# Kernel optimization log

Measured on AMD Instinct MI355X. Metric: run time of the kernel, lower is better.

Reference implementation:

```python
import jax, jax.numpy as jnp
import numpy as np

B = 1024
D = 768          # 2 * hidden_size
HID = 384        # hidden_size (split point for mu/sigma)
MLP_H = 300      # InfoNCE hidden size
LOG2PI = float(np.log(2.0 * np.pi))


def setup_inputs() -> dict:
    key = jax.random.key(0)
    ks = jax.random.split(key, 12)
    s = 0.02
    return {
        "zl": jax.random.normal(ks[0], (B, 20, D), jnp.float32),
        "zv": jax.random.normal(ks[1], (B, 36, D), jnp.float32),
        "fc_l_w": jax.random.normal(ks[2], (20,), jnp.float32) * s,
        "fc_l_b": jax.random.normal(ks[3], (), jnp.float32) * s,
        "fc_v_w": jax.random.normal(ks[4], (36,), jnp.float32) * s,
        "fc_v_b": jax.random.normal(ks[5], (), jnp.float32) * s,
        "W1": jax.random.normal(ks[6], (MLP_H, 2 * HID), jnp.float32) * s,
        "b1": jnp.zeros((MLP_H,), jnp.float32),
        "W2": jax.random.normal(ks[7], (1, MLP_H), jnp.float32) * s,
        "b2": jnp.zeros((1,), jnp.float32),
        "eps1": jax.random.normal(ks[8], (B, HID), jnp.float32),
        "eps2": jax.random.normal(ks[9], (B, HID), jnp.float32),
        "perm": jax.random.permutation(ks[10], B),
    }


def _log_prob(mu, sigma, x):
    # Independent(Normal(mu, sigma), 1).log_prob(x)
    z = (x - mu) / sigma
    return jnp.sum(-jnp.log(sigma) - 0.5 * LOG2PI - 0.5 * z * z, axis=-1)


def reference(zl, zv, fc_l_w, fc_l_b, fc_v_w, fc_v_b, W1, b1, W2, b2, eps1, eps2, perm):
    # fc over token dim: permute(0,2,1) @ Linear(20->1) -> [B, D]
    z1 = jnp.einsum('bsd,s->bd', zl, fc_l_w) + fc_l_b
    z2 = jnp.einsum('bsd,s->bd', zv, fc_v_w) + fc_v_b

    mu1, sig1 = z1[:, :HID], jax.nn.softplus(z1[:, HID:]) + 1e-7
    mu2, sig2 = z2[:, :HID], jax.nn.softplus(z2[:, HID:]) + 1e-7

    # rsample
    s1 = mu1 + sig1 * eps1  # [B, HID]
    s2 = mu2 + sig2 * eps2

    kl_1_2 = _log_prob(mu1, sig1, s1) - _log_prob(mu2, sig2, s1)
    kl_2_1 = _log_prob(mu2, sig2, s2) - _log_prob(mu1, sig1, s2)
    d_skl = jnp.mean(kl_1_2 + kl_2_1) / 2.0

    # InfoNCE(x=s1, y=s2): F(x,y) = softplus(relu([x,y]W1^T + b1) W2^T + b2)
    W1x, W1y = W1[:, :HID], W1[:, HID:]
    Ax = s1 @ W1x.T            # [B, MLP_H], x contribution
    By = s2 @ W1y.T            # [B, MLP_H], y contribution
    w2 = W2[0]                 # [MLP_H]

    # T0: matched pairs
    T0 = jax.nn.softplus(jax.nn.relu(Ax + By + b1) @ w2 + b2[0])  # [B]

    # T1[i, j] = F(x_j, y_perm[i]); tile via broadcasting instead of repeat+cat
    By_p = By[perm]                                             # [B, MLP_H]
    h = jax.nn.relu(Ax[None, :, :] + By_p[:, None, :] + b1)     # [B, B, MLP_H]
    T1 = jax.nn.softplus(h @ w2 + b2[0])                        # [B, B]

    lower_bound = T0.mean() - (jax.scipy.special.logsumexp(T1, axis=1).mean() - jnp.log(jnp.float32(B)))
    return d_skl - lower_bound
```

## Files before the change

### kernel.cpp

```cpp
#include <hip/hip_runtime.h>
#include <math.h>

#define BB   1024
#define DD   768
#define HIDV 384
#define MLPH 300
#define MLPP 320

typedef float v2f __attribute__((ext_vector_type(2)));

__device__ __forceinline__ float softplusf(float x) {
    return (x > 20.f) ? x : log1pf(expf(x));
}

__global__ void k_init(float* __restrict__ ws) {
    int i = blockIdx.x * 256 + threadIdx.x;
    if (i < 16 + BB) ws[i] = 0.f;
}

__global__ __launch_bounds__(192, 3) void k_rs(
    const float* __restrict__ zl, const float* __restrict__ zv,
    const float* __restrict__ wl, const float* __restrict__ blp,
    const float* __restrict__ wv, const float* __restrict__ bvp,
    const float* __restrict__ eps1, const float* __restrict__ eps2,
    float* __restrict__ s1, float* __restrict__ s2, float* __restrict__ accum)
{
    __shared__ float SG[768];
    __shared__ float pr[3];
    int tid = threadIdx.x;
    int b = blockIdx.x;

    const float4* zl4 = (const float4*)(zl + (size_t)b * 15360) + tid;
    const float4* zv4 = (const float4*)(zv + (size_t)b * 27648) + tid;

    float a1[4] = {0.f, 0.f, 0.f, 0.f};
    float a2[4] = {0.f, 0.f, 0.f, 0.f};

    #pragma unroll
    for (int s = 0; s < 20; ++s) {
        float4 v = zl4[s * 192];
        float w = wl[s];
        a1[0] = fmaf(v.x, w, a1[0]);
        a1[1] = fmaf(v.y, w, a1[1]);
        a1[2] = fmaf(v.z, w, a1[2]);
        a1[3] = fmaf(v.w, w, a1[3]);
    }
    #pragma unroll
    for (int s = 0; s < 36; ++s) {
        float4 v = zv4[s * 192];
        float w = wv[s];
        a2[0] = fmaf(v.x, w, a2[0]);
        a2[1] = fmaf(v.y, w, a2[1]);
        a2[2] = fmaf(v.z, w, a2[2]);
        a2[3] = fmaf(v.w, w, a2[3]);
    }

    float bl = blp[0], bv = bvp[0];

    if (tid >= 96) {
        float o1[4], o2[4];
        #pragma unroll
        for (int j = 0; j < 4; ++j) {
            o1[j] = softplusf(a1[j] + bl) + 1e-7f;
            o2[j] = softplusf(a2[j] + bv) + 1e-7f;
        }
        *(float4*)(SG + (tid - 96) * 4)       = make_float4(o1[0], o1[1], o1[2], o1[3]);
        *(float4*)(SG + 384 + (tid - 96) * 4) = make_float4(o2[0], o2[1], o2[2], o2[3]);
    }
    __syncthreads();

    float con = 0.f;
    if (tid < 96) {
        float4 e1v = ((const float4*)eps1)[b * 96 + tid];
        float4 e2v = ((const float4*)eps2)[b * 96 + tid];
        float e1a[4] = {e1v.x, e1v.y, e1v.z, e1v.w};
        float e2a[4] = {e2v.x, e2v.y, e2v.z, e2v.w};
        float4 g1 = *(const float4*)(SG + tid * 4);
        float4 g2 = *(const float4*)(SG + 384 + tid * 4);
        float g1a[4] = {g1.x, g1.y, g1.z, g1.w};
        float g2a[4] = {g2.x, g2.y, g2.z, g2.w};
        float s1o[4], s2o[4];
        #pragma unroll
        for (int j = 0; j < 4; ++j) {
            float mu1 = a1[j] + bl;
            float mu2 = a2[j] + bv;
            float sg1 = g1a[j], sg2 = g2a[j];
            float e1 = e1a[j], e2 = e2a[j];
            float sv1 = fmaf(sg1, e1, mu1);
            float sv2 = fmaf(sg2, e2, mu2);
            s1o[j] = sv1; s2o[j] = sv2;
            float z12 = (sv1 - mu2) / sg2;
            float z21 = (sv2 - mu1) / sg1;
            con += -0.5f * (e1 * e1 + e2 * e2) + 0.5f * z12 * z12 + 0.5f * z21 * z21;
        }
        ((float4*)s1)[b * 96 + tid] = make_float4(s1o[0], s1o[1], s1o[2], s1o[3]);
        ((float4*)s2)[b * 96 + tid] = make_float4(s2o[0], s2o[1], s2o[2], s2o[3]);
    }

    #pragma unroll
    for (int m = 1; m < 64; m <<= 1) con += __shfl_xor(con, m);
    if ((tid & 63) == 0) pr[tid >> 6] = con;
    __syncthreads();
    if (tid == 0) atomicAdd(&accum[0], pr[0] + pr[1] + pr[2]);
}

__global__ __launch_bounds__(256) void k_gemm(
    const float* __restrict__ s1, const float* __restrict__ s2,
    const float* __restrict__ W1, const float* __restrict__ b1,
    float* __restrict__ Axb, float* __restrict__ By)
{
    __shared__ __align__(16) float Ss[32][36];
    __shared__ __align__(16) float Ws[32][68];
    int z = blockIdx.z;
    const float* S = z ? s2 : s1;
    float* Out = z ? By : Axb;
    int wofs = z ? HIDV : 0;
    int b0 = blockIdx.x * 32;
    int k0 = blockIdx.y * 64;
    int tid = threadIdx.x;
    int srow = tid >> 3, sc = tid & 7;
    int wrow = tid >> 2, wc = tid & 3;
    int krow = k0 + wrow;
    int tx = tid & 15, ty = tid >> 4;

    float4 ps, pw[2];
    auto ld = [&](int hc) {
        ps = *(const float4*)&S[(b0 + srow) * HIDV + hc + sc * 4];
        #pragma unroll
        for (int u = 0; u < 2; ++u)
            pw[u] = (krow < MLPH) ? *(const float4*)&W1[krow * DD + wofs + hc + wc * 4 + u * 16]
                                  : make_float4(0.f, 0.f, 0.f, 0.f);
    };
    ld(0);
    v2f acc[2][2];
    acc[0][0] = (v2f){0.f, 0.f}; acc[0][1] = (v2f){0.f, 0.f};
    acc[1][0] = (v2f){0.f, 0.f}; acc[1][1] = (v2f){0.f, 0.f};

    for (int ch = 0; ch < 12; ++ch) {
        __syncthreads();
        Ss[sc * 4 + 0][srow] = ps.x; Ss[sc * 4 + 1][srow] = ps.y;
        Ss[sc * 4 + 2][srow] = ps.z; Ss[sc * 4 + 3][srow] = ps.w;
        #pragma unroll
        for (int u = 0; u < 2; ++u) {
            int hb = wc * 4 + u * 16;
            Ws[hb + 0][wrow] = pw[u].x; Ws[hb + 1][wrow] = pw[u].y;
            Ws[hb + 2][wrow] = pw[u].z; Ws[hb + 3][wrow] = pw[u].w;
        }
        __syncthreads();
        if (ch < 11) ld((ch + 1) * 32);
        #pragma unroll
        for (int h = 0; h < 32; ++h) {
            v2f sv = *(const v2f*)&Ss[h][ty * 2];
            float4 wq = *(const float4*)&Ws[h][tx * 4];
            v2f w0 = (v2f){wq.x, wq.y};
            v2f w1 = (v2f){wq.z, wq.w};
            v2f s0 = (v2f){sv.x, sv.x};
            v2f s1b = (v2f){sv.y, sv.y};
            acc[0][0] = __builtin_elementwise_fma(s0, w0, acc[0][0]);
            acc[0][1] = __builtin_elementwise_fma(s0, w1, acc[0][1]);
            acc[1][0] = __builtin_elementwise_fma(s1b, w0, acc[1][0]);
            acc[1][1] = __builtin_elementwise_fma(s1b, w1, acc[1][1]);
        }
    }
    #pragma unroll
    for (int i = 0; i < 2; ++i) {
        int bb = b0 + ty * 2 + i;
        float vraw[4] = {acc[i][0].x, acc[i][0].y, acc[i][1].x, acc[i][1].y};
        float o[4];
        #pragma unroll
        for (int j = 0; j < 4; ++j) {
            int k = k0 + tx * 4 + j;
            float v = vraw[j];
            if (!z) v += b1[k < MLPH ? k : 0];
            o[j] = (k < MLPH) ? v : 0.f;
        }
        *(float4*)&Out[bb * MLPP + k0 + tx * 4] = make_float4(o[0], o[1], o[2], o[3]);
    }
}

__global__ void k_t0(const float* __restrict__ Axb, const float* __restrict__ By,
                     const float* __restrict__ W2, const float* __restrict__ b2,
                     float* __restrict__ accum)
{
    int b = blockIdx.x;
    int l = threadIdx.x;
    float t = 0.f;
    for (int k = l; k < MLPH; k += 64)
        t = fmaf(fmaxf(Axb[b * MLPP + k] + By[b * MLPP + k], 0.f), W2[k], t);
    #pragma unroll
    for (int m = 1; m < 64; m <<= 1) t += __shfl_xor(t, m);
    if (l == 0) atomicAdd(&accum[1], softplusf(t + b2[0]));
}

__global__ __launch_bounds__(256) void k_pairs(
    const float* __restrict__ Axb, const float* __restrict__ By,
    const int* __restrict__ perm, const float* __restrict__ W2,
    const float* __restrict__ b2, float* __restrict__ sumexp)
{
    __shared__ __align__(16) float As[64][68];
    __shared__ __align__(16) float Bs[64][68];
    __shared__ float w2s[MLPP];
    int tid = threadIdx.x;
    int j0 = blockIdx.x * 64;
    int i0 = blockIdx.y * 64;
    for (int t = tid; t < MLPP; t += 256) w2s[t] = (t < MLPH) ? W2[t] : 0.f;
    int r = tid >> 2;
    int c4 = tid & 3;
    int tx = tid & 15, ty = tid >> 4;
    int prow = perm[i0 + r];

    float4 pa[4], pb[4];
    auto ld = [&](int kc) {
        #pragma unroll
        for (int u = 0; u < 4; ++u) {
            int kq = (c4 + 4 * u) * 4;
            pa[u] = *(const float4*)&Axb[(j0 + r) * MLPP + kc + kq];
            pb[u] = *(const float4*)&By[prow * MLPP + kc + kq];
        }
    };
    ld(0);
    v2f acc2[4][2];
    #pragma unroll
    for (int c = 0; c < 4; ++c) {
        acc2[c][0] = (v2f){0.f, 0.f};
        acc2[c][1] = (v2f){0.f, 0.f};
    }
    for (int ch = 0; ch < 5; ++ch) {
        __syncthreads();
        #pragma unroll
        for (int u = 0; u < 4; ++u) {
            int kq = (c4 + 4 * u) * 4;
            As[kq + 0][r] = pa[u].x; As[kq + 1][r] = pa[u].y;
            As[kq + 2][r] = pa[u].z; As[kq + 3][r] = pa[u].w;
            Bs[kq + 0][r] = pb[u].x; Bs[kq + 1][r] = pb[u].y;
            Bs[kq + 2][r] = pb[u].z; Bs[kq + 3][r] = pb[u].w;
        }
        __syncthreads();
        if (ch < 4) ld((ch + 1) * 64);
        int kc = ch * 64;
        #pragma unroll
        for (int k = 0; k < 64; ++k) {
            float w = w2s[kc + k];
            v2f wv2 = (v2f){w, w};
            float4 af = *(const float4*)&As[k][tx * 4];
            float4 bf = *(const float4*)&Bs[k][ty * 4];
            v2f a2[2] = { (v2f){af.x, af.y}, (v2f){af.z, af.w} };
            float bs[4] = {bf.x, bf.y, bf.z, bf.w};
            #pragma unroll
            for (int c = 0; c < 4; ++c) {
                v2f bc = (v2f){bs[c], bs[c]};
                #pragma unroll
                for (int d2 = 0; d2 < 2; ++d2) {
                    v2f tv = a2[d2] + bc;
                    tv = __builtin_elementwise_max(tv, (v2f){0.f, 0.f});
                    acc2[c][d2] = __builtin_elementwise_fma(tv, wv2, acc2[c][d2]);
                }
            }
        }
    }
    float b2v = b2[0];
    #pragma unroll
    for (int c = 0; c < 4; ++c) {
        float vv[4] = {acc2[c][0].x, acc2[c][0].y, acc2[c][1].x, acc2[c][1].y};
        float ssum = 0.f;
        #pragma unroll
        for (int d = 0; d < 4; ++d)
            ssum += 1.f + expf(vv[d] + b2v);
        ssum += __shfl_xor(ssum, 1);
        ssum += __shfl_xor(ssum, 2);
        ssum += __shfl_xor(ssum, 4);
        ssum += __shfl_xor(ssum, 8);
        if (tx == 0) atomicAdd(&sumexp[i0 + ty * 4 + c], ssum);
    }
}

__global__ __launch_bounds__(256) void k_final(
    const float* __restrict__ accum, const float* __restrict__ sumexp,
    float* __restrict__ out)
{
    int tid = threadIdx.x;
    float s = 0.f;
    for (int i = tid; i < BB; i += 256) s += logf(sumexp[i]);
    #pragma unroll
    for (int m = 1; m < 64; m <<= 1) s += __shfl_xor(s, m);
    __shared__ float red[4];
    if ((tid & 63) == 0) red[tid >> 6] = s;
    __syncthreads();
    if (tid == 0) {
        float lse_mean = (red[0] + red[1] + red[2] + red[3]) / (float)BB;
        float d_skl = accum[0] / (2.f * (float)BB);
        float t0_mean = accum[1] / (float)BB;
        float lower = t0_mean - (lse_mean - logf((float)BB));
        out[0] = d_skl - lower;
    }
}

extern "C" void kernel_launch(void* const* d_in, const int* in_sizes, int n_in,
                              void* d_out, int out_size, void* d_ws, size_t ws_size,
                              hipStream_t stream)
{
    const float* zl     = (const float*)d_in[0];
    const float* zv     = (const float*)d_in[1];
    const float* fc_l_w = (const float*)d_in[2];
    const float* fc_l_b = (const float*)d_in[3];
    const float* fc_v_w = (const float*)d_in[4];
    const float* fc_v_b = (const float*)d_in[5];
    const float* W1     = (const float*)d_in[6];
    const float* b1     = (const float*)d_in[7];
    const float* W2     = (const float*)d_in[8];
    const float* b2     = (const float*)d_in[9];
    const float* eps1   = (const float*)d_in[10];
    const float* eps2   = (const float*)d_in[11];
    const int*   perm   = (const int*)d_in[12];
    float* out = (float*)d_out;

    float* ws     = (float*)d_ws;
    float* accum  = ws;
    float* sumexp = ws + 16;
    float* s1     = ws + 16 + BB;
    float* s2     = s1 + BB * HIDV;
    float* Axb    = s2 + BB * HIDV;
    float* By     = Axb + BB * MLPP;

    k_init<<<5, 256, 0, stream>>>(ws);
    k_rs<<<BB, 192, 0, stream>>>(zl, zv, fc_l_w, fc_l_b, fc_v_w, fc_v_b,
                                 eps1, eps2, s1, s2, accum);
    k_gemm<<<dim3(32, 5, 2), 256, 0, stream>>>(s1, s2, W1, b1, Axb, By);
    k_t0<<<BB, 64, 0, stream>>>(Axb, By, W2, b2, accum);
    k_pairs<<<dim3(16, 16), 256, 0, stream>>>(Axb, By, perm, W2, b2, sumexp);
    k_final<<<1, 256, 0, stream>>>(accum, sumexp, out);
}
```

Measured before the change: 310.6 us.

## Shrink tiles and split work across more threads in all kernels

```diff
diff --git a/kernel.cpp b/kernel.cpp
--- a/kernel.cpp
+++ b/kernel.cpp
@@ -18,7 +18,7 @@
     if (i < 16 + BB) ws[i] = 0.f;
 }
 
-__global__ __launch_bounds__(192, 3) void k_rs(
+__global__ __launch_bounds__(384, 6) void k_rs(
     const float* __restrict__ zl, const float* __restrict__ zv,
     const float* __restrict__ wl, const float* __restrict__ blp,
     const float* __restrict__ wv, const float* __restrict__ bvp,
@@ -26,64 +26,89 @@
     float* __restrict__ s1, float* __restrict__ s2, float* __restrict__ accum)
 {
     __shared__ float SG[768];
-    __shared__ float pr[3];
+    __shared__ float MU2[384];
+    __shared__ float pr[6];
     int tid = threadIdx.x;
     int b = blockIdx.x;
-
-    const float4* zl4 = (const float4*)(zl + (size_t)b * 15360) + tid;
-    const float4* zv4 = (const float4*)(zv + (size_t)b * 27648) + tid;
-
-    float a1[4] = {0.f, 0.f, 0.f, 0.f};
-    float a2[4] = {0.f, 0.f, 0.f, 0.f};
-
-    #pragma unroll
-    for (int s = 0; s < 20; ++s) {
-        float4 v = zl4[s * 192];
-        float w = wl[s];
-        a1[0] = fmaf(v.x, w, a1[0]);
-        a1[1] = fmaf(v.y, w, a1[1]);
-        a1[2] = fmaf(v.z, w, a1[2]);
-        a1[3] = fmaf(v.w, w, a1[3]);
-    }
-    #pragma unroll
-    for (int s = 0; s < 36; ++s) {
-        float4 v = zv4[s * 192];
-        float w = wv[s];
-        a2[0] = fmaf(v.x, w, a2[0]);
-        a2[1] = fmaf(v.y, w, a2[1]);
-        a2[2] = fmaf(v.z, w, a2[2]);
-        a2[3] = fmaf(v.w, w, a2[3]);
+    int g = tid / 96;
+    int c = tid - g * 96;
+
+    const float4* p;
+    if (g < 2) p = (const float4*)(zl + (size_t)b * 15360) + ((g & 1) * 96 + c);
+    else       p = (const float4*)(zv + (size_t)b * 27648) + ((g & 1) * 96 + c);
+
+    float acc[4] = {0.f, 0.f, 0.f, 0.f};
+    if (g < 2) {
+        #pragma unroll
+        for (int t0 = 0; t0 < 20; t0 += 10) {
+            float4 vb[10];
+            #pragma unroll
+            for (int u = 0; u < 10; ++u) vb[u] = p[(t0 + u) * 192];
+            #pragma unroll
+            for (int u = 0; u < 10; ++u) {
+                float w = wl[t0 + u];
+                acc[0] = fmaf(vb[u].x, w, acc[0]);
+                acc[1] = fmaf(vb[u].y, w, acc[1]);
+                acc[2] = fmaf(vb[u].z, w, acc[2]);
+                acc[3] = fmaf(vb[u].w, w, acc[3]);
+            }
+        }
+    } else {
+        #pragma unroll
+        for (int t0 = 0; t0 < 36; t0 += 9) {
+            float4 vb[9];
+            #pragma unroll
+            for (int u = 0; u < 9; ++u) vb[u] = p[(t0 + u) * 192];
+            #pragma unroll
+            for (int u = 0; u < 9; ++u) {
+                float w = wv[t0 + u];
+                acc[0] = fmaf(vb[u].x, w, acc[0]);
+                acc[1] = fmaf(vb[u].y, w, acc[1]);
+                acc[2] = fmaf(vb[u].z, w, acc[2]);
+                acc[3] = fmaf(vb[u].w, w, acc[3]);
+            }
+        }
     }
 
     float bl = blp[0], bv = bvp[0];
 
-    if (tid >= 96) {
-        float o1[4], o2[4];
-        #pragma unroll
-        for (int j = 0; j < 4; ++j) {
-            o1[j] = softplusf(a1[j] + bl) + 1e-7f;
-            o2[j] = softplusf(a2[j] + bv) + 1e-7f;
-        }
-        *(float4*)(SG + (tid - 96) * 4)       = make_float4(o1[0], o1[1], o1[2], o1[3]);
-        *(float4*)(SG + 384 + (tid - 96) * 4) = make_float4(o2[0], o2[1], o2[2], o2[3]);
+    if (g == 1) {
+        float4 o;
+        o.x = softplusf(acc[0] + bl) + 1e-7f;
+        o.y = softplusf(acc[1] + bl) + 1e-7f;
+        o.z = softplusf(acc[2] + bl) + 1e-7f;
+        o.w = softplusf(acc[3] + bl) + 1e-7f;
+        *(float4*)(SG + c * 4) = o;
+    } else if (g == 2) {
+        *(float4*)(MU2 + c * 4) =
+            make_float4(acc[0] + bv, acc[1] + bv, acc[2] + bv, acc[3] + bv);
+    } else if (g == 3) {
+        float4 o;
+        o.x = softplusf(acc[0] + bv) + 1e-7f;
+        o.y = softplusf(acc[1] + bv) + 1e-7f;
+        o.z = softplusf(acc[2] + bv) + 1e-7f;
+        o.w = softplusf(acc[3] + bv) + 1e-7f;
+        *(float4*)(SG + 384 + c * 4) = o;
     }
     __syncthreads();
 
     float con = 0.f;
-    if (tid < 96) {
-        float4 e1v = ((const float4*)eps1)[b * 96 + tid];
-        float4 e2v = ((const float4*)eps2)[b * 96 + tid];
+    if (g == 0) {
+        float4 e1v = ((const float4*)eps1)[b * 96 + c];
+        float4 e2v = ((const float4*)eps2)[b * 96 + c];
+        float4 g1 = *(const float4*)(SG + c * 4);
+        float4 m2 = *(const float4*)(MU2 + c * 4);
+        float4 g2 = *(const float4*)(SG + 384 + c * 4);
         float e1a[4] = {e1v.x, e1v.y, e1v.z, e1v.w};
         float e2a[4] = {e2v.x, e2v.y, e2v.z, e2v.w};
-        float4 g1 = *(const float4*)(SG + tid * 4);
-        float4 g2 = *(const float4*)(SG + 384 + tid * 4);
         float g1a[4] = {g1.x, g1.y, g1.z, g1.w};
         float g2a[4] = {g2.x, g2.y, g2.z, g2.w};
+        float m2a[4] = {m2.x, m2.y, m2.z, m2.w};
         float s1o[4], s2o[4];
         #pragma unroll
         for (int j = 0; j < 4; ++j) {
-            float mu1 = a1[j] + bl;
-            float mu2 = a2[j] + bv;
+            float mu1 = acc[j] + bl;
+            float mu2 = m2a[j];
             float sg1 = g1a[j], sg2 = g2a[j];
             float e1 = e1a[j], e2 = e2a[j];
             float sv1 = fmaf(sg1, e1, mu1);
@@ -93,15 +118,16 @@
             float z21 = (sv2 - mu1) / sg1;
             con += -0.5f * (e1 * e1 + e2 * e2) + 0.5f * z12 * z12 + 0.5f * z21 * z21;
         }
-        ((float4*)s1)[b * 96 + tid] = make_float4(s1o[0], s1o[1], s1o[2], s1o[3]);
-        ((float4*)s2)[b * 96 + tid] = make_float4(s2o[0], s2o[1], s2o[2], s2o[3]);
+        ((float4*)s1)[b * 96 + c] = make_float4(s1o[0], s1o[1], s1o[2], s1o[3]);
+        ((float4*)s2)[b * 96 + c] = make_float4(s2o[0], s2o[1], s2o[2], s2o[3]);
     }
 
     #pragma unroll
     for (int m = 1; m < 64; m <<= 1) con += __shfl_xor(con, m);
     if ((tid & 63) == 0) pr[tid >> 6] = con;
     __syncthreads();
-    if (tid == 0) atomicAdd(&accum[0], pr[0] + pr[1] + pr[2]);
+    if (tid == 0)
+        atomicAdd(&accum[0], pr[0] + pr[1] + pr[2] + pr[3] + pr[4] + pr[5]);
 }
 
 __global__ __launch_bounds__(256) void k_gemm(
@@ -109,84 +135,82 @@
     const float* __restrict__ W1, const float* __restrict__ b1,
     float* __restrict__ Axb, float* __restrict__ By)
 {
-    __shared__ __align__(16) float Ss[32][36];
-    __shared__ __align__(16) float Ws[32][68];
+    __shared__ __align__(16) float Ss[32][38];
+    __shared__ __align__(16) float Ws[32][38];
     int z = blockIdx.z;
     const float* S = z ? s2 : s1;
     float* Out = z ? By : Axb;
     int wofs = z ? HIDV : 0;
     int b0 = blockIdx.x * 32;
-    int k0 = blockIdx.y * 64;
-    int tid = threadIdx.x;
-    int srow = tid >> 3, sc = tid & 7;
-    int wrow = tid >> 2, wc = tid & 3;
-    int krow = k0 + wrow;
+    int k0 = blockIdx.y * 32;
+    int tid = threadIdx.x;
+    int row = tid >> 3, q = tid & 7;
+    int krow = k0 + row;
     int tx = tid & 15, ty = tid >> 4;
 
-    float4 ps, pw[2];
+    float4 ps, pw;
     auto ld = [&](int hc) {
-        ps = *(const float4*)&S[(b0 + srow) * HIDV + hc + sc * 4];
-        #pragma unroll
-        for (int u = 0; u < 2; ++u)
-            pw[u] = (krow < MLPH) ? *(const float4*)&W1[krow * DD + wofs + hc + wc * 4 + u * 16]
-                                  : make_float4(0.f, 0.f, 0.f, 0.f);
+        ps = *(const float4*)&S[(b0 + row) * HIDV + hc + q * 4];
+        pw = (krow < MLPH) ? *(const float4*)&W1[krow * DD + wofs + hc + q * 4]
+                           : make_float4(0.f, 0.f, 0.f, 0.f);
     };
     ld(0);
-    v2f acc[2][2];
-    acc[0][0] = (v2f){0.f, 0.f}; acc[0][1] = (v2f){0.f, 0.f};
-    acc[1][0] = (v2f){0.f, 0.f}; acc[1][1] = (v2f){0.f, 0.f};
+    v2f acc[2];
+    acc[0] = (v2f){0.f, 0.f}; acc[1] = (v2f){0.f, 0.f};
 
     for (int ch = 0; ch < 12; ++ch) {
         __syncthreads();
-        Ss[sc * 4 + 0][srow] = ps.x; Ss[sc * 4 + 1][srow] = ps.y;
-        Ss[sc * 4 + 2][srow] = ps.z; Ss[sc * 4 + 3][srow] = ps.w;
-        #pragma unroll
-        for (int u = 0; u < 2; ++u) {
-            int hb = wc * 4 + u * 16;
-            Ws[hb + 0][wrow] = pw[u].x; Ws[hb + 1][wrow] = pw[u].y;
-            Ws[hb + 2][wrow] = pw[u].z; Ws[hb + 3][wrow] = pw[u].w;
-        }
+        Ss[q * 4 + 0][row] = ps.x; Ss[q * 4 + 1][row] = ps.y;
+        Ss[q * 4 + 2][row] = ps.z; Ss[q * 4 + 3][row] = ps.w;
+        Ws[q * 4 + 0][row] = pw.x; Ws[q * 4 + 1][row] = pw.y;
+        Ws[q * 4 + 2][row] = pw.z; Ws[q * 4 + 3][row] = pw.w;
         __syncthreads();
         if (ch < 11) ld((ch + 1) * 32);
         #pragma unroll
         for (int h = 0; h < 32; ++h) {
             v2f sv = *(const v2f*)&Ss[h][ty * 2];
-            float4 wq = *(const float4*)&Ws[h][tx * 4];
-            v2f w0 = (v2f){wq.x, wq.y};
-            v2f w1 = (v2f){wq.z, wq.w};
-            v2f s0 = (v2f){sv.x, sv.x};
-            v2f s1b = (v2f){sv.y, sv.y};
-            acc[0][0] = __builtin_elementwise_fma(s0, w0, acc[0][0]);
-            acc[0][1] = __builtin_elementwise_fma(s0, w1, acc[0][1]);
-            acc[1][0] = __builtin_elementwise_fma(s1b, w0, acc[1][0]);
-            acc[1][1] = __builtin_elementwise_fma(s1b, w1, acc[1][1]);
+            v2f wq = *(const v2f*)&Ws[h][tx * 2];
+            acc[0] = __builtin_elementwise_fma((v2f){sv.x, sv.x}, wq, acc[0]);
+            acc[1] = __builtin_elementwise_fma((v2f){sv.y, sv.y}, wq, acc[1]);
         }
     }
     #pragma unroll
     for (int i = 0; i < 2; ++i) {
         int bb = b0 + ty * 2 + i;
-        float vraw[4] = {acc[i][0].x, acc[i][0].y, acc[i][1].x, acc[i][1].y};
-        float o[4];
-        #pragma unroll
-        for (int j = 0; j < 4; ++j) {
-            int k = k0 + tx * 4 + j;
-            float v = vraw[j];
-            if (!z) v += b1[k < MLPH ? k : 0];
-            o[j] = (k < MLPH) ? v : 0.f;
-        }
-        *(float4*)&Out[bb * MLPP + k0 + tx * 4] = make_float4(o[0], o[1], o[2], o[3]);
-    }
-}
-
-__global__ void k_t0(const float* __restrict__ Axb, const float* __restrict__ By,
-                     const float* __restrict__ W2, const float* __restrict__ b2,
-                     float* __restrict__ accum)
-{
-    int b = blockIdx.x;
-    int l = threadIdx.x;
+        int k = k0 + tx * 2;
+        float r0 = 0.f, r1 = 0.f;
+        if (k < MLPH)     r0 = acc[i].x + (z ? 0.f : b1[k]);
+        if (k + 1 < MLPH) r1 = acc[i].y + (z ? 0.f : b1[k + 1]);
+        *(v2f*)&Out[bb * MLPP + k] = (v2f){r0, r1};
+    }
+}
+
+__global__ __launch_bounds__(256) void k_t0(
+    const float* __restrict__ Axb, const float* __restrict__ By,
+    const float* __restrict__ W2, const float* __restrict__ b2,
+    float* __restrict__ accum)
+{
+    int tid = threadIdx.x;
+    int w = tid >> 6, l = tid & 63;
+    int b = blockIdx.x * 4 + w;
+    const float4* A4 = (const float4*)(Axb + b * MLPP);
+    const float4* B4 = (const float4*)(By + b * MLPP);
+    const float4* W4 = (const float4*)W2;
     float t = 0.f;
-    for (int k = l; k < MLPH; k += 64)
-        t = fmaf(fmaxf(Axb[b * MLPP + k] + By[b * MLPP + k], 0.f), W2[k], t);
+    {
+        float4 a = A4[l], bb = B4[l], ww = W4[l];
+        t = fmaf(fmaxf(a.x + bb.x, 0.f), ww.x, t);
+        t = fmaf(fmaxf(a.y + bb.y, 0.f), ww.y, t);
+        t = fmaf(fmaxf(a.z + bb.z, 0.f), ww.z, t);
+        t = fmaf(fmaxf(a.w + bb.w, 0.f), ww.w, t);
+    }
+    if (l < 11) {
+        float4 a = A4[64 + l], bb = B4[64 + l], ww = W4[64 + l];
+        t = fmaf(fmaxf(a.x + bb.x, 0.f), ww.x, t);
+        t = fmaf(fmaxf(a.y + bb.y, 0.f), ww.y, t);
+        t = fmaf(fmaxf(a.z + bb.z, 0.f), ww.z, t);
+        t = fmaf(fmaxf(a.w + bb.w, 0.f), ww.w, t);
+    }
     #pragma unroll
     for (int m = 1; m < 64; m <<= 1) t += __shfl_xor(t, m);
     if (l == 0) atomicAdd(&accum[1], softplusf(t + b2[0]));
@@ -197,43 +221,41 @@
     const int* __restrict__ perm, const float* __restrict__ W2,
     const float* __restrict__ b2, float* __restrict__ sumexp)
 {
-    __shared__ __align__(16) float As[64][68];
-    __shared__ __align__(16) float Bs[64][68];
+    __shared__ __align__(16) float As[64][38];
+    __shared__ __align__(16) float Bs[64][38];
     __shared__ float w2s[MLPP];
     int tid = threadIdx.x;
-    int j0 = blockIdx.x * 64;
-    int i0 = blockIdx.y * 64;
+    int j0 = blockIdx.x * 32;
+    int i0 = blockIdx.y * 32;
     for (int t = tid; t < MLPP; t += 256) w2s[t] = (t < MLPH) ? W2[t] : 0.f;
-    int r = tid >> 2;
-    int c4 = tid & 3;
+    int jj = tid >> 3;
+    int kk = tid & 7;
     int tx = tid & 15, ty = tid >> 4;
-    int prow = perm[i0 + r];
-
-    float4 pa[4], pb[4];
+    int prow = perm[i0 + jj];
+
+    float4 pa[2], pb[2];
     auto ld = [&](int kc) {
         #pragma unroll
-        for (int u = 0; u < 4; ++u) {
-            int kq = (c4 + 4 * u) * 4;
-            pa[u] = *(const float4*)&Axb[(j0 + r) * MLPP + kc + kq];
+        for (int u = 0; u < 2; ++u) {
+            int kq = (kk + u * 8) * 4;
+            pa[u] = *(const float4*)&Axb[(j0 + jj) * MLPP + kc + kq];
             pb[u] = *(const float4*)&By[prow * MLPP + kc + kq];
         }
     };
     ld(0);
-    v2f acc2[4][2];
-    #pragma unroll
-    for (int c = 0; c < 4; ++c) {
-        acc2[c][0] = (v2f){0.f, 0.f};
-        acc2[c][1] = (v2f){0.f, 0.f};
-    }
+    v2f acc2[2];
+    acc2[0] = (v2f){0.f, 0.f};
+    acc2[1] = (v2f){0.f, 0.f};
+
     for (int ch = 0; ch < 5; ++ch) {
         __syncthreads();
         #pragma unroll
-        for (int u = 0; u < 4; ++u) {
-            int kq = (c4 + 4 * u) * 4;
-            As[kq + 0][r] = pa[u].x; As[kq + 1][r] = pa[u].y;
-            As[kq + 2][r] = pa[u].z; As[kq + 3][r] = pa[u].w;
-            Bs[kq + 0][r] = pb[u].x; Bs[kq + 1][r] = pb[u].y;
-            Bs[kq + 2][r] = pb[u].z; Bs[kq + 3][r] = pb[u].w;
+        for (int u = 0; u < 2; ++u) {
+            int kq = (kk + u * 8) * 4;
+            As[kq + 0][jj] = pa[u].x; As[kq + 1][jj] = pa[u].y;
+            As[kq + 2][jj] = pa[u].z; As[kq + 3][jj] = pa[u].w;
+            Bs[kq + 0][jj] = pb[u].x; Bs[kq + 1][jj] = pb[u].y;
+            Bs[kq + 2][jj] = pb[u].z; Bs[kq + 3][jj] = pb[u].w;
         }
         __syncthreads();
         if (ch < 4) ld((ch + 1) * 64);
@@ -242,35 +264,26 @@
         for (int k = 0; k < 64; ++k) {
             float w = w2s[kc + k];
             v2f wv2 = (v2f){w, w};
-            float4 af = *(const float4*)&As[k][tx * 4];
-            float4 bf = *(const float4*)&Bs[k][ty * 4];
-            v2f a2[2] = { (v2f){af.x, af.y}, (v2f){af.z, af.w} };
-            float bs[4] = {bf.x, bf.y, bf.z, bf.w};
-            #pragma unroll
-            for (int c = 0; c < 4; ++c) {
-                v2f bc = (v2f){bs[c], bs[c]};
-                #pragma unroll
-                for (int d2 = 0; d2 < 2; ++d2) {
-                    v2f tv = a2[d2] + bc;
-                    tv = __builtin_elementwise_max(tv, (v2f){0.f, 0.f});
-                    acc2[c][d2] = __builtin_elementwise_fma(tv, wv2, acc2[c][d2]);
-                }
-            }
+            v2f av = *(const v2f*)&As[k][tx * 2];
+            float b0v = Bs[k][ty * 2];
+            float b1v = Bs[k][ty * 2 + 1];
+            v2f t0v = av + (v2f){b0v, b0v};
+            t0v = __builtin_elementwise_max(t0v, (v2f){0.f, 0.f});
+            acc2[0] = __builtin_elementwise_fma(t0v, wv2, acc2[0]);
+            v2f t1v = av + (v2f){b1v, b1v};
+            t1v = __builtin_elementwise_max(t1v, (v2f){0.f, 0.f});
+            acc2[1] = __builtin_elementwise_fma(t1v, wv2, acc2[1]);
         }
     }
     float b2v = b2[0];
     #pragma unroll
-    for (int c = 0; c < 4; ++c) {
-        float vv[4] = {acc2[c][0].x, acc2[c][0].y, acc2[c][1].x, acc2[c][1].y};
-        float ssum = 0.f;
-        #pragma unroll
-        for (int d = 0; d < 4; ++d)
-            ssum += 1.f + expf(vv[d] + b2v);
+    for (int i2 = 0; i2 < 2; ++i2) {
+        float ssum = (1.f + expf(acc2[i2].x + b2v)) + (1.f + expf(acc2[i2].y + b2v));
         ssum += __shfl_xor(ssum, 1);
         ssum += __shfl_xor(ssum, 2);
         ssum += __shfl_xor(ssum, 4);
         ssum += __shfl_xor(ssum, 8);
-        if (tx == 0) atomicAdd(&sumexp[i0 + ty * 4 + c], ssum);
+        if (tx == 0) atomicAdd(&sumexp[i0 + ty * 2 + i2], ssum);
     }
 }
 
@@ -323,10 +336,10 @@
     float* By     = Axb + BB * MLPP;
 
     k_init<<<5, 256, 0, stream>>>(ws);
-    k_rs<<<BB, 192, 0, stream>>>(zl, zv, fc_l_w, fc_l_b, fc_v_w, fc_v_b,
+    k_rs<<<BB, 384, 0, stream>>>(zl, zv, fc_l_w, fc_l_b, fc_v_w, fc_v_b,
                                  eps1, eps2, s1, s2, accum);
-    k_gemm<<<dim3(32, 5, 2), 256, 0, stream>>>(s1, s2, W1, b1, Axb, By);
-    k_t0<<<BB, 64, 0, stream>>>(Axb, By, W2, b2, accum);
-    k_pairs<<<dim3(16, 16), 256, 0, stream>>>(Axb, By, perm, W2, b2, sumexp);
+    k_gemm<<<dim3(32, 10, 2), 256, 0, stream>>>(s1, s2, W1, b1, Axb, By);
+    k_t0<<<256, 256, 0, stream>>>(Axb, By, W2, b2, accum);
+    k_pairs<<<dim3(32, 32), 256, 0, stream>>>(Axb, By, perm, W2, b2, sumexp);
     k_final<<<1, 256, 0, stream>>>(accum, sumexp, out);
 }
```

Result: slower. 335.1 us (+7.9%).
